# Kernel tuning notes

Measured on AMD Instinct MI355X. Metric: run time of the kernel, lower is better.

Reference implementation:

```python
import jax, jax.numpy as jnp
import numpy as np


def setup_inputs() -> dict:
    key = jax.random.key(0)
    k1, k2 = jax.random.split(key)
    x = jax.random.normal(k1, (32, 256, 56, 56), dtype=jnp.float32)
    conv_w = jax.random.normal(k2, (1, 2, 7, 7), dtype=jnp.float32) * 0.1
    return {"x": x, "conv_w": conv_w}


def reference(x, conv_w):
    # channel-wise mean and max, keepdim -> [B,1,H,W] each
    avg_out = jnp.mean(x, axis=1, keepdims=True)
    max_out = jnp.max(x, axis=1, keepdims=True)
    y = jnp.concatenate([avg_out, max_out], axis=1)  # [B,2,H,W]
    pad = (conv_w.shape[-1] - 1) // 2
    y = jax.lax.conv_general_dilated(
        y, conv_w,
        window_strides=(1, 1),
        padding=[(pad, pad), (pad, pad)],
        dimension_numbers=("NCHW", "OIHW", "NCHW"),
    )  # [B,1,H,W]
    y = jax.nn.sigmoid(y)
    return x * y
```

## Files before the change

### kernel.cpp

```cpp
#include <hip/hip_runtime.h>
#include <math.h>

#define BN   32
#define CN   256
#define HN   56
#define WN   56
#define HWN  (HN * WN)
#define HW4  (HWN / 4)
#define CHW4 (CN * HW4)
#define NPOS (BN * HWN)
#define NQ   (NPOS / 4)
#define SPAN 64
#define NBLK (NQ / SPAN)

typedef float f32x4 __attribute__((ext_vector_type(4)));


__global__ __launch_bounds__(512) void sa_reduce_kernel(const f32x4* __restrict__ x4,
                                                        f32x4* __restrict__ avg4,
                                                        f32x4* __restrict__ mx4) {
    __shared__ f32x4 s_sum[8][SPAN];
    __shared__ f32x4 s_max[8][SPAN];

    int t = threadIdx.x;
    int j = t & 63;
    int w = t >> 6;

    int q  = blockIdx.x * SPAN + j;
    int b  = q / HW4;
    int s4 = q - b * HW4;
    const f32x4* xp = x4 + (size_t)b * CHW4 + (size_t)(w * 32) * HW4 + s4;

    f32x4 sum = {0.0f, 0.0f, 0.0f, 0.0f};
    f32x4 m   = {-INFINITY, -INFINITY, -INFINITY, -INFINITY};
#pragma unroll 8
    for (int k = 0; k < 32; ++k) {
        f32x4 v = xp[(size_t)k * HW4];
        sum += v;
        m.x = fmaxf(m.x, v.x);
        m.y = fmaxf(m.y, v.y);
        m.z = fmaxf(m.z, v.z);
        m.w = fmaxf(m.w, v.w);
    }
    s_sum[w][j] = sum;
    s_max[w][j] = m;
    __syncthreads();

    if (t < SPAN) {
        f32x4 sa = s_sum[0][t];
        f32x4 ma = s_max[0][t];
#pragma unroll
        for (int p = 1; p < 8; ++p) {
            sa += s_sum[p][t];
            f32x4 mp = s_max[p][t];
            ma.x = fmaxf(ma.x, mp.x);
            ma.y = fmaxf(ma.y, mp.y);
            ma.z = fmaxf(ma.z, mp.z);
            ma.w = fmaxf(ma.w, mp.w);
        }
        int qq = blockIdx.x * SPAN + t;
        avg4[qq] = sa * (1.0f / (float)CN);
        mx4[qq]  = ma;
    }
}

__global__ __launch_bounds__(256) void sa_conv_kernel(const float* __restrict__ avg,
                                                      const float* __restrict__ mx,
                                                      const float* __restrict__ cw,
                                                      float* __restrict__ att) {
    int p = blockIdx.x * blockDim.x + threadIdx.x;
    if (p >= NPOS) return;
    int b = p / HWN;
    int s = p - b * HWN;
    int h = s / WN;
    int w = s - h * WN;
    const float* a0 = avg + b * HWN;
    const float* m0 = mx + b * HWN;
    float acc = 0.0f;
#pragma unroll
    for (int kh = 0; kh < 7; ++kh) {
        int hh = h + kh - 3;
        if (hh < 0 || hh >= HN) continue;
#pragma unroll
        for (int kw = 0; kw < 7; ++kw) {
            int ww = w + kw - 3;
            if (ww < 0 || ww >= WN) continue;
            int idx = hh * WN + ww;
            acc = fmaf(cw[kh * 7 + kw],      a0[idx], acc);
            acc = fmaf(cw[49 + kh * 7 + kw], m0[idx], acc);
        }
    }
    att[p] = 1.0f / (1.0f + expf(-acc));
}

__global__ __launch_bounds__(512) void sa_mul_kernel(const f32x4* __restrict__ x4,
                                                     const f32x4* __restrict__ att4,
                                                     f32x4* __restrict__ out4) {
    __shared__ f32x4 s_att[SPAN];
    int t = threadIdx.x;
    int j = t & 63;
    int w = t >> 6;

    if (t < SPAN) s_att[t] = att4[blockIdx.x * SPAN + t];
    __syncthreads();

    int q  = blockIdx.x * SPAN + j;
    int b  = q / HW4;
    int s4 = q - b * HW4;
    size_t base = (size_t)b * CHW4 + (size_t)(w * 32) * HW4 + s4;

    f32x4 a = s_att[j];
#pragma unroll 8
    for (int k = 0; k < 32; ++k) {
        size_t gi = base + (size_t)k * HW4;
        f32x4 v = x4[gi];
        v.x *= a.x;
        v.y *= a.y;
        v.z *= a.z;
        v.w *= a.w;
        __builtin_nontemporal_store(v, out4 + gi);
    }
}

extern "C" void kernel_launch(void* const* d_in, const int* in_sizes, int n_in,
                              void* d_out, int out_size, void* d_ws, size_t ws_size,
                              hipStream_t stream) {
    const float* x  = (const float*)d_in[0];
    const float* cw = (const float*)d_in[1];
    float* out = (float*)d_out;

    float* avg = (float*)d_ws;
    float* mx  = avg + NPOS;
    float* att = mx + NPOS;

    sa_reduce_kernel<<<NBLK, 512, 0, stream>>>(
        (const f32x4*)x, (f32x4*)avg, (f32x4*)mx);

    sa_conv_kernel<<<(NPOS + 255) / 256, 256, 0, stream>>>(avg, mx, cw, att);

    sa_mul_kernel<<<NBLK, 512, 0, stream>>>(
        (const f32x4*)x, (const f32x4*)att, (f32x4*)out);
}
```

Before: 204.8 us.

## Split channel reduction into contiguous chunk partials and fuse conv into multiply

The channel reduction now gives each wavefront a contiguous 8-channel chunk of one image, reading whole channel planes linearly and writing partial sums and maxima to scratch in the output buffer. A combine kernel then reduces the 32 partials. The 7x7 conv plus sigmoid is fused into the multiply kernel, so the separate attention-map round trip goes away. The reduce launches only 256 blocks with heavy register arrays, which may limit latency hiding, and the partials add extra scratch traffic.

```diff
diff --git a/kernel.cpp b/kernel.cpp
--- a/kernel.cpp
+++ b/kernel.cpp
@@ -1,123 +1,144 @@
 #include <hip/hip_runtime.h>
 #include <math.h>
 
-#define BN   32
-#define CN   256
-#define HN   56
-#define WN   56
-#define HWN  (HN * WN)
-#define HW4  (HWN / 4)
-#define CHW4 (CN * HW4)
-#define NPOS (BN * HWN)
-#define NQ   (NPOS / 4)
-#define SPAN 64
-#define NBLK (NQ / SPAN)
+#define BN     32
+#define CN     256
+#define HN     56
+#define WN     56
+#define HWN    (HN * WN)
+#define HW4    (HWN / 4)
+#define NQB    HW4
+#define CHW4   (CN * HW4)
+#define NPOS   (BN * HWN)
+#define NQ     (NPOS / 4)
+#define CCH    8
+#define CHUNKS (CN / CCH)
+#define PQ     ((size_t)BN * CHUNKS * NQB)
+#define SPAN   64
+#define NBLK3  (NQ / SPAN)
 
 typedef float f32x4 __attribute__((ext_vector_type(4)));
 
+static __device__ __forceinline__ f32x4 max4(f32x4 a, f32x4 b) {
+    f32x4 r;
+    r.x = fmaxf(a.x, b.x); r.y = fmaxf(a.y, b.y);
+    r.z = fmaxf(a.z, b.z); r.w = fmaxf(a.w, b.w);
+    return r;
+}
 
-__global__ __launch_bounds__(512) void sa_reduce_kernel(const f32x4* __restrict__ x4,
-                                                        f32x4* __restrict__ avg4,
-                                                        f32x4* __restrict__ mx4) {
-    __shared__ f32x4 s_sum[8][SPAN];
-    __shared__ f32x4 s_max[8][SPAN];
+
+__global__ __launch_bounds__(256) void sa_reduce_lin(const f32x4* __restrict__ x4,
+                                                     f32x4* __restrict__ scratch) {
+    int t    = blockIdx.x * 256 + threadIdx.x;
+    int wv   = t >> 6;
+    int lane = t & 63;
+    int b     = wv >> 5;
+    int chunk = wv & 31;
+
+    const f32x4* xp = x4 + (size_t)b * CHW4 + (size_t)(chunk * CCH) * NQB;
+
+    f32x4 sum[13], mx[13];
+#pragma unroll
+    for (int i = 0; i < 13; ++i) {
+        sum[i] = (f32x4){0.0f, 0.0f, 0.0f, 0.0f};
+        mx[i]  = (f32x4){-INFINITY, -INFINITY, -INFINITY, -INFINITY};
+    }
+
+    for (int cc = 0; cc < CCH; ++cc) {
+        const f32x4* cp = xp + (size_t)cc * NQB;
+#pragma unroll
+        for (int i = 0; i < 13; ++i) {
+            int q = i * 64 + lane;
+            if (q < NQB) {
+                f32x4 v = cp[q];
+                sum[i] += v;
+                mx[i] = max4(mx[i], v);
+            }
+        }
+    }
+
+    f32x4* sumP = scratch;
+    f32x4* maxP = scratch + PQ;
+    size_t pb = (size_t)(b * CHUNKS + chunk) * NQB;
+#pragma unroll
+    for (int i = 0; i < 13; ++i) {
+        int q = i * 64 + lane;
+        if (q < NQB) {
+            sumP[pb + q] = sum[i];
+            maxP[pb + q] = mx[i];
+        }
+    }
+}
+
+__global__ __launch_bounds__(256) void sa_combine(const f32x4* __restrict__ scratch,
+                                                  f32x4* __restrict__ avg4,
+                                                  f32x4* __restrict__ mx4) {
+    int qq = blockIdx.x * 256 + threadIdx.x;
+    int b = qq / NQB;
+    int s = qq - b * NQB;
+    const f32x4* sumP = scratch + (size_t)(b * CHUNKS) * NQB + s;
+    const f32x4* maxP = sumP + PQ;
+
+    f32x4 sum = {0.0f, 0.0f, 0.0f, 0.0f};
+    f32x4 m   = {-INFINITY, -INFINITY, -INFINITY, -INFINITY};
+#pragma unroll 8
+    for (int k = 0; k < CHUNKS; ++k) {
+        sum += sumP[(size_t)k * NQB];
+        m = max4(m, maxP[(size_t)k * NQB]);
+    }
+    avg4[qq] = sum * (1.0f / (float)CN);
+    mx4[qq]  = m;
+}
+
+__global__ __launch_bounds__(512) void sa_convmul(const f32x4* __restrict__ x4,
+                                                  const float* __restrict__ avg,
+                                                  const float* __restrict__ mxp,
+                                                  const float* __restrict__ cw,
+                                                  f32x4* __restrict__ out4) {
+    __shared__ __align__(16) float s_att[SPAN * 4];
 
     int t = threadIdx.x;
+
+    if (t < SPAN * 4) {
+        int p  = blockIdx.x * (SPAN * 4) + t;
+        int bb = p / HWN;
+        int s  = p - bb * HWN;
+        int h  = s / WN;
+        int w0 = s - h * WN;
+        const float* a0 = avg + bb * HWN;
+        const float* m0 = mxp + bb * HWN;
+        float acc = 0.0f;
+#pragma unroll
+        for (int kh = 0; kh < 7; ++kh) {
+            int hh = h + kh - 3;
+            if (hh < 0 || hh >= HN) continue;
+#pragma unroll
+            for (int kw = 0; kw < 7; ++kw) {
+                int ww = w0 + kw - 3;
+                if (ww < 0 || ww >= WN) continue;
+                int idx = hh * WN + ww;
+                acc = fmaf(cw[kh * 7 + kw],      a0[idx], acc);
+                acc = fmaf(cw[49 + kh * 7 + kw], m0[idx], acc);
+            }
+        }
+        s_att[t] = 1.0f / (1.0f + expf(-acc));
+    }
+    __syncthreads();
+
     int j = t & 63;
     int w = t >> 6;
 
     int q  = blockIdx.x * SPAN + j;
     int b  = q / HW4;
     int s4 = q - b * HW4;
-    const f32x4* xp = x4 + (size_t)b * CHW4 + (size_t)(w * 32) * HW4 + s4;
-
-    f32x4 sum = {0.0f, 0.0f, 0.0f, 0.0f};
-    f32x4 m   = {-INFINITY, -INFINITY, -INFINITY, -INFINITY};
-#pragma unroll 8
-    for (int k = 0; k < 32; ++k) {
-        f32x4 v = xp[(size_t)k * HW4];
-        sum += v;
-        m.x = fmaxf(m.x, v.x);
-        m.y = fmaxf(m.y, v.y);
-        m.z = fmaxf(m.z, v.z);
-        m.w = fmaxf(m.w, v.w);
-    }
-    s_sum[w][j] = sum;
-    s_max[w][j] = m;
-    __syncthreads();
-
-    if (t < SPAN) {
-        f32x4 sa = s_sum[0][t];
-        f32x4 ma = s_max[0][t];
-#pragma unroll
-        for (int p = 1; p < 8; ++p) {
-            sa += s_sum[p][t];
-            f32x4 mp = s_max[p][t];
-            ma.x = fmaxf(ma.x, mp.x);
-            ma.y = fmaxf(ma.y, mp.y);
-            ma.z = fmaxf(ma.z, mp.z);
-            ma.w = fmaxf(ma.w, mp.w);
-        }
-        int qq = blockIdx.x * SPAN + t;
-        avg4[qq] = sa * (1.0f / (float)CN);
-        mx4[qq]  = ma;
-    }
-}
-
-__global__ __launch_bounds__(256) void sa_conv_kernel(const float* __restrict__ avg,
-                                                      const float* __restrict__ mx,
-                                                      const float* __restrict__ cw,
-                                                      float* __restrict__ att) {
-    int p = blockIdx.x * blockDim.x + threadIdx.x;
-    if (p >= NPOS) return;
-    int b = p / HWN;
-    int s = p - b * HWN;
-    int h = s / WN;
-    int w = s - h * WN;
-    const float* a0 = avg + b * HWN;
-    const float* m0 = mx + b * HWN;
-    float acc = 0.0f;
-#pragma unroll
-    for (int kh = 0; kh < 7; ++kh) {
-        int hh = h + kh - 3;
-        if (hh < 0 || hh >= HN) continue;
-#pragma unroll
-        for (int kw = 0; kw < 7; ++kw) {
-            int ww = w + kw - 3;
-            if (ww < 0 || ww >= WN) continue;
-            int idx = hh * WN + ww;
-            acc = fmaf(cw[kh * 7 + kw],      a0[idx], acc);
-            acc = fmaf(cw[49 + kh * 7 + kw], m0[idx], acc);
-        }
-    }
-    att[p] = 1.0f / (1.0f + expf(-acc));
-}
-
-__global__ __launch_bounds__(512) void sa_mul_kernel(const f32x4* __restrict__ x4,
-                                                     const f32x4* __restrict__ att4,
-                                                     f32x4* __restrict__ out4) {
-    __shared__ f32x4 s_att[SPAN];
-    int t = threadIdx.x;
-    int j = t & 63;
-    int w = t >> 6;
-
-    if (t < SPAN) s_att[t] = att4[blockIdx.x * SPAN + t];
-    __syncthreads();
-
-    int q  = blockIdx.x * SPAN + j;
-    int b  = q / HW4;
-    int s4 = q - b * HW4;
     size_t base = (size_t)b * CHW4 + (size_t)(w * 32) * HW4 + s4;
 
-    f32x4 a = s_att[j];
+    f32x4 a = *(const f32x4*)&s_att[j * 4];
 #pragma unroll 8
     for (int k = 0; k < 32; ++k) {
         size_t gi = base + (size_t)k * HW4;
         f32x4 v = x4[gi];
-        v.x *= a.x;
-        v.y *= a.y;
-        v.z *= a.z;
-        v.w *= a.w;
+        v.x *= a.x; v.y *= a.y; v.z *= a.z; v.w *= a.w;
         __builtin_nontemporal_store(v, out4 + gi);
     }
 }
@@ -131,13 +152,12 @@
 
     float* avg = (float*)d_ws;
     float* mx  = avg + NPOS;
-    float* att = mx + NPOS;
 
-    sa_reduce_kernel<<<NBLK, 512, 0, stream>>>(
-        (const f32x4*)x, (f32x4*)avg, (f32x4*)mx);
+    sa_reduce_lin<<<256, 256, 0, stream>>>((const f32x4*)x, (f32x4*)out);
 
-    sa_conv_kernel<<<(NPOS + 255) / 256, 256, 0, stream>>>(avg, mx, cw, att);
+    sa_combine<<<NQ / 256, 256, 0, stream>>>((const f32x4*)out,
+                                             (f32x4*)avg, (f32x4*)mx);
 
-    sa_mul_kernel<<<NBLK, 512, 0, stream>>>(
-        (const f32x4*)x, (const f32x4*)att, (f32x4*)out);
+    sa_convmul<<<NBLK3, 512, 0, stream>>>((const f32x4*)x, avg, mx, cw,
+                                          (f32x4*)out);
 }
```

New measurement: 213.3 us. +4.1%, slower.
